# Kernel optimization log

Measured on AMD Instinct MI355X. Metric: run time of the kernel, lower is better.

## Reference

```python
import jax, jax.numpy as jnp
import numpy as np

ALPHA = 0.2
NEG_BIG = -9e15

def setup_inputs() -> dict:
    key = jax.random.key(0)
    k1, k2, k3, k4 = jax.random.split(key, 4)
    B, N, F = 8, 2048, 256
    h = jax.random.normal(k1, (B, N, F), dtype=jnp.float32)
    adj = jax.random.randint(k2, (B, N, N), 0, 2, dtype=jnp.int32)
    W = jax.random.normal(k3, (F, F), dtype=jnp.float32) * (1.414 / jnp.sqrt(F))
    a = jax.random.normal(k4, (2 * F, 1), dtype=jnp.float32) * 0.1
    return {"h": h, "adj": adj, "W": W, "a": a}

def reference(h, adj, W, a):
    F_out = W.shape[1]
    Wh = jnp.einsum('bnf,fo->bno', h, W)            # [B,N,F]
    Wh1 = Wh @ a[:F_out]                             # [B,N,1]
    Wh2 = Wh @ a[F_out:]                             # [B,N,1]
    e = jax.nn.leaky_relu(Wh1 + jnp.swapaxes(Wh2, 1, 2), negative_slope=ALPHA)  # [B,N,N]
    scores = jnp.where(adj > 0, e, NEG_BIG)
    attention = jax.nn.softmax(scores, axis=-1)      # [B,N,N]
    h_prime = jnp.einsum('bnm,bmf->bnf', attention, Wh)
    out = h + jax.nn.elu(h_prime)                    # concat=True -> elu; residual add
    return (out, attention)
```

## Files before the change

kernel.cpp:

```cpp
#include <hip/hip_runtime.h>

#define NB 8
#define NN 2048
#define NF 256

typedef __attribute__((ext_vector_type(8))) short bf16x8;
typedef __attribute__((ext_vector_type(4))) float f32x4;

__device__ __forceinline__ unsigned short f2bf(float x) {
  union { float f; unsigned int i; } c; c.f = x;
  unsigned int r = c.i + 0x7FFFu + ((c.i >> 16) & 1u);
  return (unsigned short)(r >> 16);
}
__device__ __forceinline__ unsigned short f2bf_fast(float x) {
  union { float f; unsigned int i; } c; c.f = x;
  return (unsigned short)((c.i + 0x8000u) >> 16);
}
__device__ __forceinline__ bf16x8 cvt8(float4 c0, float4 c1) {
  union { bf16x8 v8; unsigned short us[8]; } cu;
  cu.us[0] = f2bf_fast(c0.x); cu.us[1] = f2bf_fast(c0.y);
  cu.us[2] = f2bf_fast(c0.z); cu.us[3] = f2bf_fast(c0.w);
  cu.us[4] = f2bf_fast(c1.x); cu.us[5] = f2bf_fast(c1.y);
  cu.us[6] = f2bf_fast(c1.z); cu.us[7] = f2bf_fast(c1.w);
  return cu.v8;
}

__global__ __launch_bounds__(256) void k_prep(
    const float* __restrict__ W, const float* __restrict__ a,
    unsigned short* __restrict__ WT, float* __restrict__ u, float* __restrict__ v) {
  int t = threadIdx.x;
  if (blockIdx.x < 256) {
    int k = blockIdx.x;
    WT[t * 256 + k] = f2bf(W[k * 256 + t]);
  } else {
    float su = 0.f, sv = 0.f;
    for (int o = 0; o < 256; ++o) {
      float w = W[t * 256 + o];
      su += w * a[o];
      sv += w * a[256 + o];
    }
    u[t] = su; v[t] = sv;
  }
}

__global__ __launch_bounds__(256) void k_wht(
    const float* __restrict__ h, const unsigned short* __restrict__ WTr,
    unsigned short* __restrict__ WhT) {
  int bx = blockIdx.x;
  int b = bx >> 6;
  int t = bx & 63;
  int fBlk = (t >> 4) * 64;
  int iBlk = (t & 15) * 128;
  int wave = threadIdx.x >> 6, lane = threadIdx.x & 63;
  int fW = fBlk + (wave >> 1) * 32;
  int iW = iBlk + (wave & 1) * 64;
  int l15 = lane & 15, q8 = (lane >> 4) * 8;
  const float* hB = h + (size_t)b * NN * NF;

  f32x4 acc[2][4];
#pragma unroll
  for (int mt = 0; mt < 2; ++mt)
#pragma unroll
    for (int nt = 0; nt < 4; ++nt)
      acc[mt][nt] = (f32x4){0.f, 0.f, 0.f, 0.f};

  for (int k0 = 0; k0 < NF; k0 += 32) {
    int kk = k0 + q8;
    bf16x8 af[2], bfr[4];
#pragma unroll
    for (int mt = 0; mt < 2; ++mt) {
      int f = fW + mt * 16 + l15;
      af[mt] = *(const bf16x8*)(WTr + f * 256 + kk);
    }
#pragma unroll
    for (int nt = 0; nt < 4; ++nt) {
      int i = iW + nt * 16 + l15;
      const float* p = hB + (size_t)i * NF + kk;
      bfr[nt] = cvt8(*(const float4*)p, *(const float4*)(p + 4));
    }
#pragma unroll
    for (int mt = 0; mt < 2; ++mt)
#pragma unroll
      for (int nt = 0; nt < 4; ++nt)
        acc[mt][nt] = __builtin_amdgcn_mfma_f32_16x16x32_bf16(af[mt], bfr[nt], acc[mt][nt], 0, 0, 0);
  }

  unsigned short* WhTb = WhT + (size_t)b * NF * NN;
  int q4 = (lane >> 4) * 4;
#pragma unroll
  for (int mt = 0; mt < 2; ++mt)
#pragma unroll
    for (int nt = 0; nt < 4; ++nt)
#pragma unroll
      for (int r = 0; r < 4; ++r) {
        int f = fW + mt * 16 + q4 + r;
        int i = iW + nt * 16 + l15;
        WhTb[(size_t)f * NN + i] = f2bf(acc[mt][nt][r]);
      }
}

__global__ __launch_bounds__(256) void k_proj(
    const float* __restrict__ h, const float* __restrict__ u,
    const float* __restrict__ v, float* __restrict__ Wh1, float* __restrict__ Wh2) {
  int row = blockIdx.x * 4 + (threadIdx.x >> 6);
  int lane = threadIdx.x & 63;
  float4 hv = *(const float4*)(h + (size_t)row * NF + lane * 4);
  const float* up = u + lane * 4;
  const float* vp = v + lane * 4;
  float su = hv.x * up[0] + hv.y * up[1] + hv.z * up[2] + hv.w * up[3];
  float sv = hv.x * vp[0] + hv.y * vp[1] + hv.z * vp[2] + hv.w * vp[3];
#pragma unroll
  for (int off = 32; off >= 1; off >>= 1) {
    su += __shfl_xor(su, off);
    sv += __shfl_xor(sv, off);
  }
  if (lane == 0) { Wh1[row] = su; Wh2[row] = sv; }
}

__global__ __launch_bounds__(256) void k_attn(
    const int* __restrict__ adj, const float* __restrict__ Wh1,
    const float* __restrict__ Wh2, float* __restrict__ att) {
  const float NEGBIG = -9.0e15f;
  int wave = threadIdx.x >> 6, lane = threadIdx.x & 63;
  int row = blockIdx.x * 4 + wave;
  int b = row >> 11;
  const int* arow = adj + (size_t)row * NN;
  const float* w2 = Wh2 + ((size_t)b << 11);
  float w1 = Wh1[row];

  float s[32];
#pragma unroll
  for (int c = 0; c < 8; ++c) {
    int j = c * 256 + lane * 4;
    int4 av = *(const int4*)(arow + j);
    float4 pv = *(const float4*)(w2 + j);
    float x;
    x = w1 + pv.x; x = x >= 0.f ? x : 0.2f * x; s[c * 4 + 0] = (av.x > 0) ? x : NEGBIG;
    x = w1 + pv.y; x = x >= 0.f ? x : 0.2f * x; s[c * 4 + 1] = (av.y > 0) ? x : NEGBIG;
    x = w1 + pv.z; x = x >= 0.f ? x : 0.2f * x; s[c * 4 + 2] = (av.z > 0) ? x : NEGBIG;
    x = w1 + pv.w; x = x >= 0.f ? x : 0.2f * x; s[c * 4 + 3] = (av.w > 0) ? x : NEGBIG;
  }

  float m = s[0];
#pragma unroll
  for (int k = 1; k < 32; ++k) m = fmaxf(m, s[k]);
#pragma unroll
  for (int off = 32; off >= 1; off >>= 1) m = fmaxf(m, __shfl_xor(m, off));

  float sum = 0.f;
#pragma unroll
  for (int k = 0; k < 32; ++k) { s[k] = __expf(s[k] - m); sum += s[k]; }
#pragma unroll
  for (int off = 32; off >= 1; off >>= 1) sum += __shfl_xor(sum, off);
  float inv = 1.0f / sum;

  float* orow = att + (size_t)row * NN;
#pragma unroll
  for (int c = 0; c < 8; ++c) {
    int j = c * 256 + lane * 4;
    float4 o = make_float4(s[c * 4 + 0] * inv, s[c * 4 + 1] * inv,
                           s[c * 4 + 2] * inv, s[c * 4 + 3] * inv);
    *(float4*)(orow + j) = o;
  }
}

__global__ __launch_bounds__(256) void k_out(
    const float* __restrict__ att, const unsigned short* __restrict__ WhT,
    const float* __restrict__ h, float* __restrict__ out) {
  int bx = blockIdx.x;
  int b = bx >> 6;
  int iW = (bx & 63) * 32;
  int wave = threadIdx.x >> 6, lane = threadIdx.x & 63;
  int fW = wave * 64;
  int l15 = lane & 15, q8 = (lane >> 4) * 8;
  const float* attB = att + (size_t)b * NN * NN;
  const unsigned short* WTb = WhT + (size_t)b * NF * NN;

  f32x4 acc[2][4];
#pragma unroll
  for (int mt = 0; mt < 2; ++mt)
#pragma unroll
    for (int nt = 0; nt < 4; ++nt)
      acc[mt][nt] = (f32x4){0.f, 0.f, 0.f, 0.f};

  for (int j0 = 0; j0 < NN; j0 += 32) {
    int kk = j0 + q8;
    bf16x8 af[2], bfr[4];
#pragma unroll
    for (int mt = 0; mt < 2; ++mt) {
      int i = iW + mt * 16 + l15;
      const float* p = attB + (size_t)i * NN + kk;
      af[mt] = cvt8(*(const float4*)p, *(const float4*)(p + 4));
    }
#pragma unroll
    for (int nt = 0; nt < 4; ++nt) {
      int f = fW + nt * 16 + l15;
      bfr[nt] = *(const bf16x8*)(WTb + (size_t)f * NN + kk);
    }
#pragma unroll
    for (int mt = 0; mt < 2; ++mt)
#pragma unroll
      for (int nt = 0; nt < 4; ++nt)
        acc[mt][nt] = __builtin_amdgcn_mfma_f32_16x16x32_bf16(af[mt], bfr[nt], acc[mt][nt], 0, 0, 0);
  }

  int q4 = (lane >> 4) * 4;
#pragma unroll
  for (int mt = 0; mt < 2; ++mt)
#pragma unroll
    for (int nt = 0; nt < 4; ++nt)
#pragma unroll
      for (int r = 0; r < 4; ++r) {
        int i = iW + mt * 16 + q4 + r;
        int f = fW + nt * 16 + l15;
        size_t idx = ((size_t)(b * NN + i)) * NF + f;
        float hp = acc[mt][nt][r];
        float el = hp > 0.f ? hp : expm1f(hp);
        out[idx] = h[idx] + el;
      }
}

extern "C" void kernel_launch(void* const* d_in, const int* in_sizes, int n_in,
                              void* d_out, int out_size, void* d_ws, size_t ws_size,
                              hipStream_t stream) {
  const float* h = nullptr; const int* adj = nullptr;
  const float* W = nullptr; const float* a = nullptr;
  for (int i = 0; i < n_in; ++i) {
    int s = in_sizes[i];
    if (s == NB * NN * NF) h = (const float*)d_in[i];
    else if (s == NB * NN * NN) adj = (const int*)d_in[i];
    else if (s == NF * NF) W = (const float*)d_in[i];
    else if (s == 2 * NF) a = (const float*)d_in[i];
  }

  float* out = (float*)d_out;
  float* att = out + (size_t)NB * NN * NF;

  char* ws = (char*)d_ws;
  unsigned short* WhT = (unsigned short*)ws;
  unsigned short* WTr = (unsigned short*)(ws + 8388608);
  float* u   = (float*)(ws + 8388608 + 131072);
  float* v   = u + 256;
  float* Wh1 = v + 256;
  float* Wh2 = Wh1 + NB * NN;

  k_prep<<<257, 256, 0, stream>>>(W, a, WTr, u, v);
  k_wht<<<512, 256, 0, stream>>>(h, WTr, WhT);
  k_proj<<<NB * NN / 4, 256, 0, stream>>>(h, u, v, Wh1, Wh2);
  k_attn<<<NB * NN / 4, 256, 0, stream>>>(adj, Wh1, Wh2, att);
  k_out<<<512, 256, 0, stream>>>(att, WhT, h, out);
}
```

Before: 419.7 us.

## Fuse softmax attention with attention-times-Wh matmul via bf16 shared-memory tile

Merges the attention softmax kernel and the output GEMM into one kernel. Each block computes 16 softmax rows, writes the fp32 attention to global memory, and keeps a swizzled bf16 copy in LDS. The GEMM then reads its A operand from LDS instead of re-reading fp32 attention from HBM. This removes a 128MB read, but each block now re-streams the batch's WhT per 16 rows instead of per 32. Per-thread register pressure also rises from holding four rows of scores.

New measurement: 400.6 us. 1.05x faster.

```diff
diff --git a/kernel.cpp b/kernel.cpp
--- a/kernel.cpp
+++ b/kernel.cpp
@@ -117,107 +117,111 @@
   if (lane == 0) { Wh1[row] = su; Wh2[row] = sv; }
 }
 
-__global__ __launch_bounds__(256) void k_attn(
+__global__ __launch_bounds__(256, 2) void k_fuse(
     const int* __restrict__ adj, const float* __restrict__ Wh1,
-    const float* __restrict__ Wh2, float* __restrict__ att) {
+    const float* __restrict__ Wh2, const unsigned short* __restrict__ WhT,
+    const float* __restrict__ h, float* __restrict__ att, float* __restrict__ out) {
+  __shared__ unsigned short satt[16 * 2048];
   const float NEGBIG = -9.0e15f;
+  int bx = blockIdx.x;
+  int b = bx >> 7;
+  int i0 = (bx & 127) * 16;
   int wave = threadIdx.x >> 6, lane = threadIdx.x & 63;
-  int row = blockIdx.x * 4 + wave;
-  int b = row >> 11;
-  const int* arow = adj + (size_t)row * NN;
   const float* w2 = Wh2 + ((size_t)b << 11);
-  float w1 = Wh1[row];
-
-  float s[32];
-#pragma unroll
-  for (int c = 0; c < 8; ++c) {
-    int j = c * 256 + lane * 4;
-    int4 av = *(const int4*)(arow + j);
-    float4 pv = *(const float4*)(w2 + j);
-    float x;
-    x = w1 + pv.x; x = x >= 0.f ? x : 0.2f * x; s[c * 4 + 0] = (av.x > 0) ? x : NEGBIG;
-    x = w1 + pv.y; x = x >= 0.f ? x : 0.2f * x; s[c * 4 + 1] = (av.y > 0) ? x : NEGBIG;
-    x = w1 + pv.z; x = x >= 0.f ? x : 0.2f * x; s[c * 4 + 2] = (av.z > 0) ? x : NEGBIG;
-    x = w1 + pv.w; x = x >= 0.f ? x : 0.2f * x; s[c * 4 + 3] = (av.w > 0) ? x : NEGBIG;
-  }
-
-  float m = s[0];
-#pragma unroll
-  for (int k = 1; k < 32; ++k) m = fmaxf(m, s[k]);
-#pragma unroll
-  for (int off = 32; off >= 1; off >>= 1) m = fmaxf(m, __shfl_xor(m, off));
-
-  float sum = 0.f;
-#pragma unroll
-  for (int k = 0; k < 32; ++k) { s[k] = __expf(s[k] - m); sum += s[k]; }
-#pragma unroll
-  for (int off = 32; off >= 1; off >>= 1) sum += __shfl_xor(sum, off);
-  float inv = 1.0f / sum;
-
-  float* orow = att + (size_t)row * NN;
-#pragma unroll
-  for (int c = 0; c < 8; ++c) {
-    int j = c * 256 + lane * 4;
-    float4 o = make_float4(s[c * 4 + 0] * inv, s[c * 4 + 1] * inv,
-                           s[c * 4 + 2] * inv, s[c * 4 + 3] * inv);
-    *(float4*)(orow + j) = o;
-  }
-}
-
-__global__ __launch_bounds__(256) void k_out(
-    const float* __restrict__ att, const unsigned short* __restrict__ WhT,
-    const float* __restrict__ h, float* __restrict__ out) {
-  int bx = blockIdx.x;
-  int b = bx >> 6;
-  int iW = (bx & 63) * 32;
-  int wave = threadIdx.x >> 6, lane = threadIdx.x & 63;
+
+  float s[4][32];
+  int rowbase = b * NN + i0 + wave * 4;
+#pragma unroll
+  for (int rr = 0; rr < 4; ++rr) {
+    const int* arow = adj + (size_t)(rowbase + rr) * NN;
+    float w1 = Wh1[rowbase + rr];
+#pragma unroll
+    for (int c = 0; c < 8; ++c) {
+      int j = c * 256 + lane * 4;
+      int4 av = *(const int4*)(arow + j);
+      float4 pv = *(const float4*)(w2 + j);
+      float x;
+      x = w1 + pv.x; x = x >= 0.f ? x : 0.2f * x; s[rr][c*4+0] = (av.x > 0) ? x : NEGBIG;
+      x = w1 + pv.y; x = x >= 0.f ? x : 0.2f * x; s[rr][c*4+1] = (av.y > 0) ? x : NEGBIG;
+      x = w1 + pv.z; x = x >= 0.f ? x : 0.2f * x; s[rr][c*4+2] = (av.z > 0) ? x : NEGBIG;
+      x = w1 + pv.w; x = x >= 0.f ? x : 0.2f * x; s[rr][c*4+3] = (av.w > 0) ? x : NEGBIG;
+    }
+  }
+
+  float inv[4];
+#pragma unroll
+  for (int rr = 0; rr < 4; ++rr) {
+    float m = s[rr][0];
+#pragma unroll
+    for (int k = 1; k < 32; ++k) m = fmaxf(m, s[rr][k]);
+#pragma unroll
+    for (int off = 32; off >= 1; off >>= 1) m = fmaxf(m, __shfl_xor(m, off));
+    float sum = 0.f;
+#pragma unroll
+    for (int k = 0; k < 32; ++k) { s[rr][k] = __expf(s[rr][k] - m); sum += s[rr][k]; }
+#pragma unroll
+    for (int off = 32; off >= 1; off >>= 1) sum += __shfl_xor(sum, off);
+    inv[rr] = 1.0f / sum;
+  }
+
+#pragma unroll
+  for (int rr = 0; rr < 4; ++rr) {
+    int row_local = wave * 4 + rr;
+    int swz = row_local * 8;
+    float* orow = att + (size_t)(rowbase + rr) * NN;
+    unsigned short* srow = satt + row_local * 2048;
+    float iv = inv[rr];
+#pragma unroll
+    for (int c = 0; c < 8; ++c) {
+      int j = c * 256 + lane * 4;
+      float a0 = s[rr][c*4+0] * iv, a1 = s[rr][c*4+1] * iv;
+      float a2 = s[rr][c*4+2] * iv, a3 = s[rr][c*4+3] * iv;
+      *(float4*)(orow + j) = make_float4(a0, a1, a2, a3);
+      int e = ((j & ~7) ^ swz) + (j & 7);
+      union { short4 v4; unsigned short us[4]; } pk;
+      pk.us[0] = f2bf_fast(a0); pk.us[1] = f2bf_fast(a1);
+      pk.us[2] = f2bf_fast(a2); pk.us[3] = f2bf_fast(a3);
+      *(short4*)(srow + e) = pk.v4;
+    }
+  }
+
+  __syncthreads();
+
   int fW = wave * 64;
   int l15 = lane & 15, q8 = (lane >> 4) * 8;
-  const float* attB = att + (size_t)b * NN * NN;
   const unsigned short* WTb = WhT + (size_t)b * NF * NN;
-
-  f32x4 acc[2][4];
-#pragma unroll
-  for (int mt = 0; mt < 2; ++mt)
-#pragma unroll
-    for (int nt = 0; nt < 4; ++nt)
-      acc[mt][nt] = (f32x4){0.f, 0.f, 0.f, 0.f};
-
-  for (int j0 = 0; j0 < NN; j0 += 32) {
-    int kk = j0 + q8;
-    bf16x8 af[2], bfr[4];
-#pragma unroll
-    for (int mt = 0; mt < 2; ++mt) {
-      int i = iW + mt * 16 + l15;
-      const float* p = attB + (size_t)i * NN + kk;
-      af[mt] = cvt8(*(const float4*)p, *(const float4*)(p + 4));
-    }
+  const unsigned short* aRow = satt + l15 * 2048;
+  int swzA = l15 * 8;
+
+  f32x4 acc[4];
+#pragma unroll
+  for (int nt = 0; nt < 4; ++nt) acc[nt] = (f32x4){0.f, 0.f, 0.f, 0.f};
+
+  for (int kk = 0; kk < NN; kk += 32) {
+    bf16x8 afr = *(const bf16x8*)(aRow + (((kk + q8) ^ swzA)));
+    bf16x8 bfr[4];
 #pragma unroll
     for (int nt = 0; nt < 4; ++nt) {
       int f = fW + nt * 16 + l15;
-      bfr[nt] = *(const bf16x8*)(WTb + (size_t)f * NN + kk);
-    }
-#pragma unroll
-    for (int mt = 0; mt < 2; ++mt)
-#pragma unroll
-      for (int nt = 0; nt < 4; ++nt)
-        acc[mt][nt] = __builtin_amdgcn_mfma_f32_16x16x32_bf16(af[mt], bfr[nt], acc[mt][nt], 0, 0, 0);
+      bfr[nt] = *(const bf16x8*)(WTb + (size_t)f * NN + kk + q8);
+    }
+#pragma unroll
+    for (int nt = 0; nt < 4; ++nt)
+      acc[nt] = __builtin_amdgcn_mfma_f32_16x16x32_bf16(afr, bfr[nt], acc[nt], 0, 0, 0);
   }
 
   int q4 = (lane >> 4) * 4;
 #pragma unroll
-  for (int mt = 0; mt < 2; ++mt)
-#pragma unroll
-    for (int nt = 0; nt < 4; ++nt)
-#pragma unroll
-      for (int r = 0; r < 4; ++r) {
-        int i = iW + mt * 16 + q4 + r;
-        int f = fW + nt * 16 + l15;
-        size_t idx = ((size_t)(b * NN + i)) * NF + f;
-        float hp = acc[mt][nt][r];
-        float el = hp > 0.f ? hp : expm1f(hp);
-        out[idx] = h[idx] + el;
-      }
+  for (int nt = 0; nt < 4; ++nt)
+#pragma unroll
+    for (int r = 0; r < 4; ++r) {
+      int i = i0 + q4 + r;
+      int f = fW + nt * 16 + l15;
+      size_t idx = ((size_t)(b * NN + i)) * NF + f;
+      float hp = acc[nt][r];
+      float el = hp > 0.f ? hp : expm1f(hp);
+      out[idx] = h[idx] + el;
+    }
 }
 
 extern "C" void kernel_launch(void* const* d_in, const int* in_sizes, int n_in,
@@ -247,6 +251,5 @@
   k_prep<<<257, 256, 0, stream>>>(W, a, WTr, u, v);
   k_wht<<<512, 256, 0, stream>>>(h, WTr, WhT);
   k_proj<<<NB * NN / 4, 256, 0, stream>>>(h, u, v, Wh1, Wh2);
-  k_attn<<<NB * NN / 4, 256, 0, stream>>>(adj, Wh1, Wh2, att);
-  k_out<<<512, 256, 0, stream>>>(att, WhT, h, out);
-}
+  k_fuse<<<NB * 128, 256, 0, stream>>>(adj, Wh1, Wh2, WhT, h, att, out);
+}
```

## Fuse Wh projection into Wh GEMM via LDS staging and retile output GEMM

Applied to the files above, without the earlier changes.

The k_proj kernel is merged into the Wh transpose-GEMM. Each block now loads 16 rows of h once, computes the Wh1/Wh2 dot products, and stages bf16 h in swizzled LDS for the MFMA B operand, which removes a separate pass over h. The output GEMM is retiled to 16-row blocks with 1024 blocks and a 64-wide K step, and launch-bound occupancy hints are added to k_attn and k_out. The trade-off is that k_out now reads each WhT tile for every 16 rows instead of every 32, which doubles WhT traffic in exchange for more parallelism.

Result: slower. 467.0 us (+11.3%).

```diff
diff --git a/kernel.cpp b/kernel.cpp
--- a/kernel.cpp
+++ b/kernel.cpp
@@ -43,81 +43,103 @@
   }
 }
 
-__global__ __launch_bounds__(256) void k_wht(
+__global__ __launch_bounds__(256) void k_whtp(
     const float* __restrict__ h, const unsigned short* __restrict__ WTr,
-    unsigned short* __restrict__ WhT) {
+    const float* __restrict__ u, const float* __restrict__ v,
+    unsigned short* __restrict__ WhT, float* __restrict__ Wh1,
+    float* __restrict__ Wh2) {
+  __shared__ unsigned short hs[16 * 256];
+  __shared__ float us[256], vs[256];
   int bx = blockIdx.x;
-  int b = bx >> 6;
-  int t = bx & 63;
-  int fBlk = (t >> 4) * 64;
-  int iBlk = (t & 15) * 128;
-  int wave = threadIdx.x >> 6, lane = threadIdx.x & 63;
-  int fW = fBlk + (wave >> 1) * 32;
-  int iW = iBlk + (wave & 1) * 64;
+  int b = bx >> 7;
+  int i0 = (bx & 127) * 16;
+  int t = threadIdx.x;
+
+  us[t] = u[t]; vs[t] = v[t];
+
+  int ir = t >> 4, kg = (t & 15) * 16;
+  const float* hrow = h + ((size_t)(b * NN + i0 + ir)) * NF + kg;
+  float4 c0 = *(const float4*)(hrow);
+  float4 c1 = *(const float4*)(hrow + 4);
+  float4 c2 = *(const float4*)(hrow + 8);
+  float4 c3 = *(const float4*)(hrow + 12);
+  __syncthreads();
+
+  float su, sv;
+  {
+    const float* up = us + kg; const float* vp = vs + kg;
+    su = c0.x*up[0] + c0.y*up[1] + c0.z*up[2] + c0.w*up[3]
+       + c1.x*up[4] + c1.y*up[5] + c1.z*up[6] + c1.w*up[7]
+       + c2.x*up[8] + c2.y*up[9] + c2.z*up[10] + c2.w*up[11]
+       + c3.x*up[12] + c3.y*up[13] + c3.z*up[14] + c3.w*up[15];
+    sv = c0.x*vp[0] + c0.y*vp[1] + c0.z*vp[2] + c0.w*vp[3]
+       + c1.x*vp[4] + c1.y*vp[5] + c1.z*vp[6] + c1.w*vp[7]
+       + c2.x*vp[8] + c2.y*vp[9] + c2.z*vp[10] + c2.w*vp[11]
+       + c3.x*vp[12] + c3.y*vp[13] + c3.z*vp[14] + c3.w*vp[15];
+  }
+#pragma unroll
+  for (int off = 8; off >= 1; off >>= 1) {
+    su += __shfl_xor(su, off);
+    sv += __shfl_xor(sv, off);
+  }
+  if ((t & 15) == 0) {
+    Wh1[b * NN + i0 + ir] = su;
+    Wh2[b * NN + i0 + ir] = sv;
+  }
+
+  int swz = ir * 8;
+  unsigned short* srow = hs + ir * 256;
+  {
+    union { short4 v4; unsigned short us4[4]; } pk;
+    float4 cc[4] = {c0, c1, c2, c3};
+#pragma unroll
+    for (int q = 0; q < 4; ++q) {
+      int basek = kg + q * 4;
+      int pos = ((basek & ~7) ^ swz) + (basek & 7);
+      pk.us4[0] = f2bf_fast(cc[q].x); pk.us4[1] = f2bf_fast(cc[q].y);
+      pk.us4[2] = f2bf_fast(cc[q].z); pk.us4[3] = f2bf_fast(cc[q].w);
+      *(short4*)(srow + pos) = pk.v4;
+    }
+  }
+  __syncthreads();
+
+  int wave = t >> 6, lane = t & 63;
   int l15 = lane & 15, q8 = (lane >> 4) * 8;
-  const float* hB = h + (size_t)b * NN * NF;
-
-  f32x4 acc[2][4];
-#pragma unroll
-  for (int mt = 0; mt < 2; ++mt)
-#pragma unroll
-    for (int nt = 0; nt < 4; ++nt)
-      acc[mt][nt] = (f32x4){0.f, 0.f, 0.f, 0.f};
-
-  for (int k0 = 0; k0 < NF; k0 += 32) {
-    int kk = k0 + q8;
-    bf16x8 af[2], bfr[4];
-#pragma unroll
-    for (int mt = 0; mt < 2; ++mt) {
-      int f = fW + mt * 16 + l15;
-      af[mt] = *(const bf16x8*)(WTr + f * 256 + kk);
-    }
-#pragma unroll
-    for (int nt = 0; nt < 4; ++nt) {
-      int i = iW + nt * 16 + l15;
-      const float* p = hB + (size_t)i * NF + kk;
-      bfr[nt] = cvt8(*(const float4*)p, *(const float4*)(p + 4));
-    }
-#pragma unroll
-    for (int mt = 0; mt < 2; ++mt)
-#pragma unroll
-      for (int nt = 0; nt < 4; ++nt)
-        acc[mt][nt] = __builtin_amdgcn_mfma_f32_16x16x32_bf16(af[mt], bfr[nt], acc[mt][nt], 0, 0, 0);
+  int fW = wave * 64;
+  const unsigned short* bRow = hs + l15 * 256;
+  int swzB = l15 * 8;
+
+  f32x4 acc[4];
+#pragma unroll
+  for (int ft = 0; ft < 4; ++ft) acc[ft] = (f32x4){0.f, 0.f, 0.f, 0.f};
+
+#pragma unroll
+  for (int kk = 0; kk < NF; kk += 32) {
+    bf16x8 bfr = *(const bf16x8*)(bRow + ((kk + q8) ^ swzB));
+    bf16x8 af[4];
+#pragma unroll
+    for (int ft = 0; ft < 4; ++ft) {
+      int f = fW + ft * 16 + l15;
+      af[ft] = *(const bf16x8*)(WTr + f * 256 + kk + q8);
+    }
+#pragma unroll
+    for (int ft = 0; ft < 4; ++ft)
+      acc[ft] = __builtin_amdgcn_mfma_f32_16x16x32_bf16(af[ft], bfr, acc[ft], 0, 0, 0);
   }
 
   unsigned short* WhTb = WhT + (size_t)b * NF * NN;
   int q4 = (lane >> 4) * 4;
 #pragma unroll
-  for (int mt = 0; mt < 2; ++mt)
-#pragma unroll
-    for (int nt = 0; nt < 4; ++nt)
-#pragma unroll
-      for (int r = 0; r < 4; ++r) {
-        int f = fW + mt * 16 + q4 + r;
-        int i = iW + nt * 16 + l15;
-        WhTb[(size_t)f * NN + i] = f2bf(acc[mt][nt][r]);
-      }
-}
-
-__global__ __launch_bounds__(256) void k_proj(
-    const float* __restrict__ h, const float* __restrict__ u,
-    const float* __restrict__ v, float* __restrict__ Wh1, float* __restrict__ Wh2) {
-  int row = blockIdx.x * 4 + (threadIdx.x >> 6);
-  int lane = threadIdx.x & 63;
-  float4 hv = *(const float4*)(h + (size_t)row * NF + lane * 4);
-  const float* up = u + lane * 4;
-  const float* vp = v + lane * 4;
-  float su = hv.x * up[0] + hv.y * up[1] + hv.z * up[2] + hv.w * up[3];
-  float sv = hv.x * vp[0] + hv.y * vp[1] + hv.z * vp[2] + hv.w * vp[3];
-#pragma unroll
-  for (int off = 32; off >= 1; off >>= 1) {
-    su += __shfl_xor(su, off);
-    sv += __shfl_xor(sv, off);
-  }
-  if (lane == 0) { Wh1[row] = su; Wh2[row] = sv; }
-}
-
-__global__ __launch_bounds__(256) void k_attn(
+  for (int ft = 0; ft < 4; ++ft)
+#pragma unroll
+    for (int r = 0; r < 4; ++r) {
+      int f = fW + ft * 16 + q4 + r;
+      int i = i0 + l15;
+      WhTb[(size_t)f * NN + i] = f2bf(acc[ft][r]);
+    }
+}
+
+__global__ __launch_bounds__(256, 6) void k_attn(
     const int* __restrict__ adj, const float* __restrict__ Wh1,
     const float* __restrict__ Wh2, float* __restrict__ att) {
   const float NEGBIG = -9.0e15f;
@@ -135,10 +157,10 @@
     int4 av = *(const int4*)(arow + j);
     float4 pv = *(const float4*)(w2 + j);
     float x;
-    x = w1 + pv.x; x = x >= 0.f ? x : 0.2f * x; s[c * 4 + 0] = (av.x > 0) ? x : NEGBIG;
-    x = w1 + pv.y; x = x >= 0.f ? x : 0.2f * x; s[c * 4 + 1] = (av.y > 0) ? x : NEGBIG;
-    x = w1 + pv.z; x = x >= 0.f ? x : 0.2f * x; s[c * 4 + 2] = (av.z > 0) ? x : NEGBIG;
-    x = w1 + pv.w; x = x >= 0.f ? x : 0.2f * x; s[c * 4 + 3] = (av.w > 0) ? x : NEGBIG;
+    x = w1 + pv.x; x = x >= 0.f ? x : 0.2f * x; s[c*4+0] = (av.x > 0) ? x : NEGBIG;
+    x = w1 + pv.y; x = x >= 0.f ? x : 0.2f * x; s[c*4+1] = (av.y > 0) ? x : NEGBIG;
+    x = w1 + pv.z; x = x >= 0.f ? x : 0.2f * x; s[c*4+2] = (av.z > 0) ? x : NEGBIG;
+    x = w1 + pv.w; x = x >= 0.f ? x : 0.2f * x; s[c*4+3] = (av.w > 0) ? x : NEGBIG;
   }
 
   float m = s[0];
@@ -158,66 +180,64 @@
 #pragma unroll
   for (int c = 0; c < 8; ++c) {
     int j = c * 256 + lane * 4;
-    float4 o = make_float4(s[c * 4 + 0] * inv, s[c * 4 + 1] * inv,
-                           s[c * 4 + 2] * inv, s[c * 4 + 3] * inv);
+    float4 o = make_float4(s[c*4+0] * inv, s[c*4+1] * inv,
+                           s[c*4+2] * inv, s[c*4+3] * inv);
     *(float4*)(orow + j) = o;
   }
 }
 
-__global__ __launch_bounds__(256) void k_out(
+__global__ __launch_bounds__(256, 4) void k_out(
     const float* __restrict__ att, const unsigned short* __restrict__ WhT,
     const float* __restrict__ h, float* __restrict__ out) {
   int bx = blockIdx.x;
-  int b = bx >> 6;
-  int iW = (bx & 63) * 32;
+  int b = bx >> 7;
+  int i0 = (bx & 127) * 16;
   int wave = threadIdx.x >> 6, lane = threadIdx.x & 63;
+  int l15 = lane & 15, q8 = (lane >> 4) * 8;
   int fW = wave * 64;
-  int l15 = lane & 15, q8 = (lane >> 4) * 8;
-  const float* attB = att + (size_t)b * NN * NN;
+  const float* aRow = att + ((size_t)(b * NN + i0 + l15)) * NN;
   const unsigned short* WTb = WhT + (size_t)b * NF * NN;
 
-  f32x4 acc[2][4];
-#pragma unroll
-  for (int mt = 0; mt < 2; ++mt)
+  f32x4 acc[4];
+#pragma unroll
+  for (int nt = 0; nt < 4; ++nt) acc[nt] = (f32x4){0.f, 0.f, 0.f, 0.f};
+
+  for (int kk = 0; kk < NN; kk += 64) {
+    const float* p0 = aRow + kk + q8;
+    const float* p1 = aRow + kk + 32 + q8;
+    float4 a00 = *(const float4*)(p0);
+    float4 a01 = *(const float4*)(p0 + 4);
+    float4 a10 = *(const float4*)(p1);
+    float4 a11 = *(const float4*)(p1 + 4);
+    bf16x8 b0[4], b1[4];
+#pragma unroll
+    for (int nt = 0; nt < 4; ++nt) {
+      const unsigned short* q = WTb + (size_t)(fW + nt * 16 + l15) * NN + kk + q8;
+      b0[nt] = *(const bf16x8*)(q);
+      b1[nt] = *(const bf16x8*)(q + 32);
+    }
+    bf16x8 a0 = cvt8(a00, a01);
+    bf16x8 a1 = cvt8(a10, a11);
 #pragma unroll
     for (int nt = 0; nt < 4; ++nt)
-      acc[mt][nt] = (f32x4){0.f, 0.f, 0.f, 0.f};
-
-  for (int j0 = 0; j0 < NN; j0 += 32) {
-    int kk = j0 + q8;
-    bf16x8 af[2], bfr[4];
-#pragma unroll
-    for (int mt = 0; mt < 2; ++mt) {
-      int i = iW + mt * 16 + l15;
-      const float* p = attB + (size_t)i * NN + kk;
-      af[mt] = cvt8(*(const float4*)p, *(const float4*)(p + 4));
-    }
-#pragma unroll
-    for (int nt = 0; nt < 4; ++nt) {
+      acc[nt] = __builtin_amdgcn_mfma_f32_16x16x32_bf16(a0, b0[nt], acc[nt], 0, 0, 0);
+#pragma unroll
+    for (int nt = 0; nt < 4; ++nt)
+      acc[nt] = __builtin_amdgcn_mfma_f32_16x16x32_bf16(a1, b1[nt], acc[nt], 0, 0, 0);
+  }
+
+  int q4 = (lane >> 4) * 4;
+#pragma unroll
+  for (int nt = 0; nt < 4; ++nt)
+#pragma unroll
+    for (int r = 0; r < 4; ++r) {
+      int i = i0 + q4 + r;
       int f = fW + nt * 16 + l15;
-      bfr[nt] = *(const bf16x8*)(WTb + (size_t)f * NN + kk);
-    }
-#pragma unroll
-    for (int mt = 0; mt < 2; ++mt)
-#pragma unroll
-      for (int nt = 0; nt < 4; ++nt)
-        acc[mt][nt] = __builtin_amdgcn_mfma_f32_16x16x32_bf16(af[mt], bfr[nt], acc[mt][nt], 0, 0, 0);
-  }
-
-  int q4 = (lane >> 4) * 4;
-#pragma unroll
-  for (int mt = 0; mt < 2; ++mt)
-#pragma unroll
-    for (int nt = 0; nt < 4; ++nt)
-#pragma unroll
-      for (int r = 0; r < 4; ++r) {
-        int i = iW + mt * 16 + q4 + r;
-        int f = fW + nt * 16 + l15;
-        size_t idx = ((size_t)(b * NN + i)) * NF + f;
-        float hp = acc[mt][nt][r];
-        float el = hp > 0.f ? hp : expm1f(hp);
-        out[idx] = h[idx] + el;
-      }
+      size_t idx = ((size_t)(b * NN + i)) * NF + f;
+      float hp = acc[nt][r];
+      float el = hp > 0.f ? hp : expm1f(hp);
+      out[idx] = h[idx] + el;
+    }
 }
 
 extern "C" void kernel_launch(void* const* d_in, const int* in_sizes, int n_in,
@@ -245,8 +265,7 @@
   float* Wh2 = Wh1 + NB * NN;
 
   k_prep<<<257, 256, 0, stream>>>(W, a, WTr, u, v);
-  k_wht<<<512, 256, 0, stream>>>(h, WTr, WhT);
-  k_proj<<<NB * NN / 4, 256, 0, stream>>>(h, u, v, Wh1, Wh2);
+  k_whtp<<<NB * 128, 256, 0, stream>>>(h, WTr, u, v, WhT, Wh1, Wh2);
   k_attn<<<NB * NN / 4, 256, 0, stream>>>(adj, Wh1, Wh2, att);
-  k_out<<<512, 256, 0, stream>>>(att, WhT, h, out);
-}
+  k_out<<<NB * 128, 256, 0, stream>>>(att, WhT, h, out);
+}
```
